# Kernel tuning notes

Hardware: AMD Instinct MI355X
Metric: run time of the kernel (lower is better)

## Reference

```python
import jax, jax.numpy as jnp
import numpy as np

PATCH_NUM = 10  # self.patch_num divisor
TOP_N = 5


def _extract_patches(feat, ps):
    """feat: [1,C,H,W] -> [P, C*ps*ps] with P = (H-ps)*(W-ps), matching the
    original loop over h in range(H-ps), w in range(W-ps)."""
    C, H, W = feat.shape[1:]
    Hm, Wm = H - ps, W - ps
    shifts = [feat[0, :, i:i + Hm, j:j + Wm] for i in range(ps) for j in range(ps)]
    patches = jnp.stack(shifts, axis=1)          # [C, ps*ps, Hm, Wm]
    return patches.reshape(C * ps * ps, Hm * Wm).T  # [P, K], P index = h*Wm + w


def _scale_loss(src_f, tgt_f, pos, ps):
    C = src_f.shape[1]
    K = C * ps * ps
    patches = _extract_patches(src_f, ps)  # [P, K]

    def per_target(p):
        th, tw = p[0], p[1]
        tpatch = jax.lax.dynamic_slice(tgt_f, (0, 0, th, tw), (1, C, ps, ps)).reshape(K)
        dist = jnp.sum(jnp.abs(patches - tpatch), axis=1)  # [P] summed L1 per patch
        _, ids = jax.lax.top_k(-dist, TOP_N)                # 5 nearest patches
        sel = patches[ids]                                   # [TOP_N, K]
        # sum over top-n of mean-L1, each divided by top_n (as in original)
        return jnp.sum(jnp.mean(jnp.abs(sel - tpatch), axis=1)) / TOP_N

    # sequential map over the small number of target patches keeps peak memory
    # at one [P,K] abs-diff buffer per step
    return jnp.sum(jax.lax.map(per_target, pos))


def setup_inputs() -> dict:
    key = jax.random.key(0)
    k0, k1, k2, k3, k4, k5 = jax.random.split(key, 6)
    return {
        "src_f0": jax.random.normal(k0, (1, 64, 256, 256), dtype=jnp.float32),
        "tgt_f0": jax.random.normal(k1, (1, 64, 256, 256), dtype=jnp.float32),
        "src_f1": jax.random.normal(k2, (1, 128, 128, 128), dtype=jnp.float32),
        "tgt_f1": jax.random.normal(k3, (1, 128, 128, 128), dtype=jnp.float32),
        "pos0": jax.random.randint(k4, (10, 2), 0, 253, dtype=jnp.int32),
        "pos1": jax.random.randint(k5, (5, 2), 0, 127, dtype=jnp.int32),
    }


def reference(src_f0, tgt_f0, src_f1, tgt_f1, pos0, pos1):
    loss = _scale_loss(src_f0, tgt_f0, pos0, 3) + _scale_loss(src_f1, tgt_f1, pos1, 1)
    return loss / PATCH_NUM
```

## Files before the change

kernel.cpp:

```cpp
#include <hip/hip_runtime.h>
#include <hip/hip_bf16.h>

#define BIG 3.4e38f


__device__ __forceinline__ void merge5(float a[5], const float* b) {
    float r[5];
#pragma unroll
    for (int k = 0; k < 5; ++k) {
        float best = BIG;
#pragma unroll
        for (int i = 0; i <= k + 1; ++i) {
            const int j = k + 1 - i;
            float va = (i == 0) ? -BIG : a[i - 1];
            float vb = (j == 0) ? -BIG : b[j - 1];
            best = fminf(best, fmaxf(va, vb));
        }
        r[k] = best;
    }
#pragma unroll
    for (int k = 0; k < 5; ++k) a[k] = r[k];
}

__device__ __forceinline__ void top5_insert(float m[5], float d) {
    if (d < m[4]) {
        m[4] = d;
#pragma unroll
        for (int k = 4; k > 0; --k) {
            float lo = fminf(m[k - 1], m[k]);
            float hi = fmaxf(m[k - 1], m[k]);
            m[k - 1] = lo;
            m[k] = hi;
        }
    }
}

__device__ __forceinline__ void wave_merge_top5(float m[5]) {
#pragma unroll
    for (int off = 1; off < 64; off <<= 1) {
        float o[5];
#pragma unroll
        for (int k = 0; k < 5; ++k) o[k] = __shfl_xor(m[k], off, 64);
        merge5(m, o);
    }
}

__device__ __forceinline__ bool block_merge_top5(float m[5], float (*s_top)[5],
                                                 float r[5]) {
    const int wid = threadIdx.x >> 6;
    if ((threadIdx.x & 63) == 0) {
#pragma unroll
        for (int k = 0; k < 5; ++k) s_top[wid][k] = m[k];
    }
    __syncthreads();
    if (threadIdx.x == 0) {
#pragma unroll
        for (int k = 0; k < 5; ++k) r[k] = s_top[0][k];
        merge5(r, s_top[1]);
        merge5(r, s_top[2]);
        merge5(r, s_top[3]);
        return true;
    }
    return false;
}

__global__ __launch_bounds__(256) void dist_all_kernel(
    const float* __restrict__ src0, const float* __restrict__ tgt0,
    const int* __restrict__ pos0, const float* __restrict__ src1,
    const float* __restrict__ tgt1, const int* __restrict__ pos1,
    float* __restrict__ dist0, float* __restrict__ p2b) {
    __shared__ float tl[960];
    __shared__ float s_top[4][5];

    if (blockIdx.y < 8) {
        constexpr int H = 256, W = 256, HW = H * W, T = 10, CCH = 8;
        constexpr int PLANE = 253 * 256;
        const int c0 = blockIdx.y * CCH;

        for (int idx = threadIdx.x; idx < T * CCH * 9; idx += 256) {
            int t = idx / (CCH * 9);
            int rem = idx - t * (CCH * 9);
            int cc = rem / 9;
            int r2 = rem - cc * 9;
            int i = r2 / 3, j = r2 - i * 3;
            int th = pos0[2 * t], tw = pos0[2 * t + 1];
            tl[((t * CCH + cc) * 3 + i) * 4 + j] =
                tgt0[(size_t)(c0 + cc) * HW + (th + i) * W + (tw + j)];
        }
        __syncthreads();

        const int tx = threadIdx.x >> 2;
        const int ty = threadIdx.x & 3;
        const int h = blockIdx.x;
        const int w0 = tx * 4;
        const int bw = (w0 <= 248) ? w0 + 4 : 250;

        float acc[T][4];
#pragma unroll
        for (int t = 0; t < T; ++t)
#pragma unroll
            for (int n = 0; n < 4; ++n) acc[t][n] = 0.f;

        const float* sb = src0 + (size_t)(c0 + ty * 2) * HW + h * W;
#pragma unroll
        for (int ccl = 0; ccl < 2; ++ccl) {
            const float* row0 = sb + (size_t)ccl * HW;
            const int cc = ty * 2 + ccl;
#pragma unroll
            for (int i = 0; i < 3; ++i) {
                const float4 a = *(const float4*)(row0 + i * W + w0);
                const float2 b = *(const float2*)(row0 + i * W + bw);
                const float r[6] = {a.x, a.y, a.z, a.w, b.x, b.y};
#pragma unroll
                for (int t = 0; t < T; ++t) {
                    const float4 tv =
                        *(const float4*)&tl[((t * CCH + cc) * 3 + i) * 4];
#pragma unroll
                    for (int n = 0; n < 4; ++n)
                        acc[t][n] += fabsf(r[n] - tv.x) +
                                     fabsf(r[n + 1] - tv.y) +
                                     fabsf(r[n + 2] - tv.z);
                }
            }
        }

#pragma unroll
        for (int t = 0; t < T; ++t)
#pragma unroll
            for (int n = 0; n < 4; ++n) {
                float v = acc[t][n];
                v += __shfl_xor(v, 1, 64);
                v += __shfl_xor(v, 2, 64);
                acc[t][n] = v;
            }
        if (ty == 0) {
            float* dp = dist0 + (size_t)blockIdx.y * T * PLANE + h * 256 + w0;
#pragma unroll
            for (int t = 0; t < T; ++t) {
                float4 o = {acc[t][0], acc[t][1], acc[t][2], acc[t][3]};
                *(float4*)(dp + (size_t)t * PLANE) = o;
            }
        }
    } else {
        if (blockIdx.x >= 64) return;
        constexpr int H = 128, W = 128, HW = H * W, T = 5, C = 128;
        for (int idx = threadIdx.x; idx < T * C; idx += 256) {
            int t = idx / C, cc = idx - t * C;
            tl[idx] =
                tgt1[(size_t)cc * HW + pos1[2 * t] * W + pos1[2 * t + 1]];
        }
        __syncthreads();

        const int w = threadIdx.x & 127;
        const int h = blockIdx.x * 2 + (threadIdx.x >> 7);
        float acc[T] = {0.f, 0.f, 0.f, 0.f, 0.f};
        const float* sp = src1 + h * W + w;
        for (int cc = 0; cc < C; ++cc) {
            const float v = sp[(size_t)cc * HW];
#pragma unroll
            for (int t = 0; t < T; ++t) acc[t] += fabsf(v - tl[t * C + cc]);
        }
        const bool valid = (h < 127) && (w < 127);
#pragma unroll
        for (int t = 0; t < T; ++t) {
            float m[5] = {valid ? acc[t] : BIG, BIG, BIG, BIG, BIG};
            wave_merge_top5(m);
            float r[5];
            if (block_merge_top5(m, s_top, r)) {
                float* dst = p2b + (t * 64 + blockIdx.x) * 5;
#pragma unroll
                for (int k = 0; k < 5; ++k) dst[k] = r[k];
            }
            __syncthreads();
        }
    }
}

template <int PLANE, int ROWW, int VALIDW, int NCH, int T, int NB>
__global__ __launch_bounds__(256) void top5_stage_kernel(
    const float* __restrict__ dist, float* __restrict__ part2) {
    __shared__ float s_top[4][5];
    const int t = blockIdx.y;
    constexpr int NF = PLANE / 4;
    constexpr int ITERS = (NF + NB * 256 - 1) / (NB * 256);
    float m[5] = {BIG, BIG, BIG, BIG, BIG};
#pragma unroll
    for (int k = 0; k < ITERS; ++k) {
        const int f = blockIdx.x * (ITERS * 256) + k * 256 + threadIdx.x;
        if (f < NF) {
            float4 s = *(const float4*)&dist[(size_t)t * PLANE + f * 4];
#pragma unroll
            for (int ch = 1; ch < NCH; ++ch) {
                float4 u =
                    *(const float4*)&dist[((size_t)ch * T + t) * PLANE + f * 4];
                s.x += u.x; s.y += u.y; s.z += u.z; s.w += u.w;
            }
            const int w0 = (f * 4) & (ROWW - 1);
            top5_insert(m, (w0 + 0 < VALIDW) ? s.x : BIG);
            top5_insert(m, (w0 + 1 < VALIDW) ? s.y : BIG);
            top5_insert(m, (w0 + 2 < VALIDW) ? s.z : BIG);
            top5_insert(m, (w0 + 3 < VALIDW) ? s.w : BIG);
        }
    }
    wave_merge_top5(m);
    float r[5];
    if (block_merge_top5(m, s_top, r)) {
        float* dst = part2 + (t * NB + blockIdx.x) * 5;
#pragma unroll
        for (int k = 0; k < 5; ++k) dst[k] = r[k];
    }
}

__global__ __launch_bounds__(256) void final_merge_kernel(
    const float* __restrict__ p2a, int na,
    const float* __restrict__ p2b, int nb,
    unsigned int* __restrict__ out) {
    __shared__ float s_sum[15];
    const int lane = threadIdx.x & 63;
    const int wv = threadIdx.x >> 6;
#pragma unroll
    for (int rt = 0; rt < 4; ++rt) {
        const int t = wv * 4 + rt;
        if (t < 15) {
            const float* base = (t < 10) ? p2a + t * na : p2b + (t - 10) * nb;
            const int n = (t < 10) ? na : nb;
            const float scale =
                (t < 10) ? 1.f / (576.f * 5.f) : 1.f / (128.f * 5.f);
            float m[5] = {BIG, BIG, BIG, BIG, BIG};
            for (int b0 = 0; b0 < n; b0 += 64)
                if (b0 + lane < n) top5_insert(m, base[b0 + lane]);
            wave_merge_top5(m);
            if (lane == 0)
                s_sum[t] = (m[0] + m[1] + m[2] + m[3] + m[4]) * scale;
        }
    }
    __syncthreads();
    if (threadIdx.x == 0) {
        float total = 0.f;
#pragma unroll
        for (int t = 0; t < 15; ++t) total += s_sum[t];
        union { float f; unsigned int i; } uf;
        uf.f = total * 0.1f;
        unsigned int bf = (uf.i + 0x7FFFu + ((uf.i >> 16) & 1u)) >> 16;
        out[0] = (uf.i & 0xFFFF0000u) | (bf & 0xFFFFu);
    }
}

template <int C, int H, int PS, int WM>
__global__ __launch_bounds__(256) void dist_top5_kernel(
    const float* __restrict__ src, const float* __restrict__ tgt,
    const int* __restrict__ pos, float* __restrict__ part) {
    constexpr int W = H;
    constexpr int K = C * PS * PS;
    constexpr int P = WM * WM;
    __shared__ float tlv[K];
    __shared__ float s_top[4][5];
    const int t = blockIdx.y;
    const int th = pos[2 * t], tw = pos[2 * t + 1];
    for (int idx = threadIdx.x; idx < K; idx += 256) {
        int c = idx / (PS * PS);
        int rem = idx - c * PS * PS;
        int i = rem / PS, j = rem - i * PS;
        tlv[idx] = tgt[(c * H + th + i) * W + tw + j];
    }
    __syncthreads();
    const int p = blockIdx.x * 256 + threadIdx.x;
    float d = BIG;
    if (p < P) {
        const int h = p / WM, w = p - h * WM;
        float acc = 0.f;
        for (int c = 0; c < C; ++c)
#pragma unroll
            for (int i = 0; i < PS; ++i) {
                const float* r = src + (c * H + h + i) * W + w;
                const float* tr = &tlv[(c * PS + i) * PS];
#pragma unroll
                for (int j = 0; j < PS; ++j) acc += fabsf(r[j] - tr[j]);
            }
        d = acc;
    }
    float m[5] = {d, BIG, BIG, BIG, BIG};
    wave_merge_top5(m);
    float r[5];
    if (block_merge_top5(m, s_top, r)) {
        float* dst = part + (t * gridDim.x + blockIdx.x) * 5;
#pragma unroll
        for (int k = 0; k < 5; ++k) dst[k] = r[k];
    }
}

extern "C" void kernel_launch(void* const* d_in, const int* in_sizes, int n_in,
                              void* d_out, int out_size, void* d_ws, size_t ws_size,
                              hipStream_t stream) {
    const float* src0 = (const float*)d_in[0];
    const float* tgt0 = (const float*)d_in[1];
    const float* src1 = (const float*)d_in[2];
    const float* tgt1 = (const float*)d_in[3];
    const int* pos0 = (const int*)d_in[4];
    const int* pos1 = (const int*)d_in[5];
    unsigned int* out = (unsigned int*)d_out;

    constexpr size_t PLANE0 = 253 * 256;
    constexpr size_t NP2A = 10 * 16 * 5;
    constexpr size_t NP2B = 5 * 64 * 5;
    const size_t need = (8 * 10 * PLANE0 + NP2A + NP2B) * 4;

    if (ws_size >= need) {
        float* dist0 = (float*)d_ws;
        float* p2a = dist0 + 8 * 10 * PLANE0;
        float* p2b = p2a + NP2A;

        dist_all_kernel<<<dim3(253, 9), 256, 0, stream>>>(
            src0, tgt0, pos0, src1, tgt1, pos1, dist0, p2b);
        top5_stage_kernel<253 * 256, 256, 253, 8, 10, 16>
            <<<dim3(16, 10), 256, 0, stream>>>(dist0, p2a);
        final_merge_kernel<<<dim3(1), 256, 0, stream>>>(p2a, 80, p2b, 320, out);
    } else {
        float* part0 = (float*)d_ws;
        float* part1 = part0 + 10 * 251 * 5;
        dist_top5_kernel<64, 256, 3, 253>
            <<<dim3(251, 10), 256, 0, stream>>>(src0, tgt0, pos0, part0);
        dist_top5_kernel<128, 128, 1, 127>
            <<<dim3(64, 5), 256, 0, stream>>>(src1, tgt1, pos1, part1);
        final_merge_kernel<<<dim3(1), 256, 0, stream>>>(part0, 1255, part1, 320, out);
    }
}
```

Before: 146.2 us.

## Split scale-0 distance work into two target passes with per-thread channel and wider columns

Scale-0 distance blocks now split the 10 targets into two passes of 5 across a doubled grid y dimension. Each thread handles one channel and 8 output columns instead of 2 channels and 4 columns. A third shuffle stage reduces across the 8 channel lanes, and launch bounds request 8 blocks per CU. The aim is more blocks and fewer accumulators per thread for better occupancy, at the cost of reading the source rows twice and doing more shuffles.

```diff
diff --git a/kernel.cpp b/kernel.cpp
--- a/kernel.cpp
+++ b/kernel.cpp
@@ -64,7 +64,7 @@
     return false;
 }
 
-__global__ __launch_bounds__(256) void dist_all_kernel(
+__global__ __launch_bounds__(256, 8) void dist_all_kernel(
     const float* __restrict__ src0, const float* __restrict__ tgt0,
     const int* __restrict__ pos0, const float* __restrict__ src1,
     const float* __restrict__ tgt1, const int* __restrict__ pos1,
@@ -72,73 +72,75 @@
     __shared__ float tl[960];
     __shared__ float s_top[4][5];
 
-    if (blockIdx.y < 8) {
-        constexpr int H = 256, W = 256, HW = H * W, T = 10, CCH = 8;
+    if (blockIdx.y < 16) {
+        constexpr int H = 256, W = 256, HW = H * W, CCH = 8;
         constexpr int PLANE = 253 * 256;
-        const int c0 = blockIdx.y * CCH;
-
-        for (int idx = threadIdx.x; idx < T * CCH * 9; idx += 256) {
-            int t = idx / (CCH * 9);
-            int rem = idx - t * (CCH * 9);
+        const int chunk = blockIdx.y & 7;
+        const int pass = blockIdx.y >> 3;
+        const int c0 = chunk * CCH;
+        const int t0 = pass * 5;
+
+        for (int idx = threadIdx.x; idx < 5 * CCH * 9; idx += 256) {
+            int tt = idx / (CCH * 9);
+            int rem = idx - tt * (CCH * 9);
             int cc = rem / 9;
             int r2 = rem - cc * 9;
             int i = r2 / 3, j = r2 - i * 3;
-            int th = pos0[2 * t], tw = pos0[2 * t + 1];
-            tl[((t * CCH + cc) * 3 + i) * 4 + j] =
+            int th = pos0[2 * (t0 + tt)], tw = pos0[2 * (t0 + tt) + 1];
+            tl[((tt * CCH + cc) * 3 + i) * 4 + j] =
                 tgt0[(size_t)(c0 + cc) * HW + (th + i) * W + (tw + j)];
         }
         __syncthreads();
 
-        const int tx = threadIdx.x >> 2;
-        const int ty = threadIdx.x & 3;
+        const int tx = threadIdx.x >> 3;
+        const int cs = threadIdx.x & 7;
         const int h = blockIdx.x;
-        const int w0 = tx * 4;
-        const int bw = (w0 <= 248) ? w0 + 4 : 250;
-
-        float acc[T][4];
-#pragma unroll
-        for (int t = 0; t < T; ++t)
-#pragma unroll
-            for (int n = 0; n < 4; ++n) acc[t][n] = 0.f;
-
-        const float* sb = src0 + (size_t)(c0 + ty * 2) * HW + h * W;
-#pragma unroll
-        for (int ccl = 0; ccl < 2; ++ccl) {
-            const float* row0 = sb + (size_t)ccl * HW;
-            const int cc = ty * 2 + ccl;
-#pragma unroll
-            for (int i = 0; i < 3; ++i) {
-                const float4 a = *(const float4*)(row0 + i * W + w0);
-                const float2 b = *(const float2*)(row0 + i * W + bw);
-                const float r[6] = {a.x, a.y, a.z, a.w, b.x, b.y};
-#pragma unroll
-                for (int t = 0; t < T; ++t) {
-                    const float4 tv =
-                        *(const float4*)&tl[((t * CCH + cc) * 3 + i) * 4];
-#pragma unroll
-                    for (int n = 0; n < 4; ++n)
-                        acc[t][n] += fabsf(r[n] - tv.x) +
-                                     fabsf(r[n + 1] - tv.y) +
-                                     fabsf(r[n + 2] - tv.z);
-                }
-            }
-        }
-
-#pragma unroll
-        for (int t = 0; t < T; ++t)
-#pragma unroll
-            for (int n = 0; n < 4; ++n) {
+        const int w0 = tx * 8;
+        const int cw = (w0 <= 246) ? w0 + 8 : 254;
+
+        float acc[5][8];
+#pragma unroll
+        for (int t = 0; t < 5; ++t)
+#pragma unroll
+            for (int n = 0; n < 8; ++n) acc[t][n] = 0.f;
+
+        const float* row = src0 + (size_t)(c0 + cs) * HW + h * W;
+#pragma unroll
+        for (int i = 0; i < 3; ++i) {
+            const float4 a = *(const float4*)(row + i * W + w0);
+            const float4 b = *(const float4*)(row + i * W + w0 + 4);
+            const float2 c = *(const float2*)(row + i * W + cw);
+            const float r[10] = {a.x, a.y, a.z, a.w, b.x,
+                                 b.y, b.z, b.w, c.x, c.y};
+#pragma unroll
+            for (int t = 0; t < 5; ++t) {
+                const float4 tv =
+                    *(const float4*)&tl[((t * CCH + cs) * 3 + i) * 4];
+#pragma unroll
+                for (int n = 0; n < 8; ++n)
+                    acc[t][n] += fabsf(r[n] - tv.x) + fabsf(r[n + 1] - tv.y) +
+                                 fabsf(r[n + 2] - tv.z);
+            }
+        }
+
+#pragma unroll
+        for (int t = 0; t < 5; ++t)
+#pragma unroll
+            for (int n = 0; n < 8; ++n) {
                 float v = acc[t][n];
                 v += __shfl_xor(v, 1, 64);
                 v += __shfl_xor(v, 2, 64);
+                v += __shfl_xor(v, 4, 64);
                 acc[t][n] = v;
             }
-        if (ty == 0) {
-            float* dp = dist0 + (size_t)blockIdx.y * T * PLANE + h * 256 + w0;
-#pragma unroll
-            for (int t = 0; t < T; ++t) {
-                float4 o = {acc[t][0], acc[t][1], acc[t][2], acc[t][3]};
-                *(float4*)(dp + (size_t)t * PLANE) = o;
+        if (cs == 0) {
+            float* dp = dist0 + ((size_t)chunk * 10 + t0) * PLANE + h * 256 + w0;
+#pragma unroll
+            for (int t = 0; t < 5; ++t) {
+                float4 o0 = {acc[t][0], acc[t][1], acc[t][2], acc[t][3]};
+                float4 o1 = {acc[t][4], acc[t][5], acc[t][6], acc[t][7]};
+                *(float4*)(dp + (size_t)t * PLANE) = o0;
+                *(float4*)(dp + (size_t)t * PLANE + 4) = o1;
             }
         }
     } else {
@@ -310,7 +312,7 @@
         float* p2a = dist0 + 8 * 10 * PLANE0;
         float* p2b = p2a + NP2A;
 
-        dist_all_kernel<<<dim3(253, 9), 256, 0, stream>>>(
+        dist_all_kernel<<<dim3(253, 17), 256, 0, stream>>>(
             src0, tgt0, pos0, src1, tgt1, pos1, dist0, p2b);
         top5_stage_kernel<253 * 256, 256, 253, 8, 10, 16>
             <<<dim3(16, 10), 256, 0, stream>>>(dist0, p2a);
```

Result: slower. 335.7 us (+129.7%).
